# Kernel optimization log

Hardware: AMD Instinct MI355X
Metric: run time of the kernel (lower is better)

The kernel has to match this reference:

```python
import jax, jax.numpy as jnp
import numpy as np

EPS = 1e-08


def setup_inputs() -> dict:
    key = jax.random.key(0)
    k1, k2 = jax.random.split(key)
    n, d = 8192, 64
    x = jax.random.normal(k1, (n, d), dtype=jnp.float32)
    y = jax.random.randint(k2, (n,), 0, 10, dtype=jnp.int64)
    # weights = 1 / temperature_init = 1 / 0.1
    weights = jnp.full((1,), 10.0, dtype=jnp.float32)
    return {"x": x, "y": y, "weights": weights}


def reference(x, y, weights):
    n = x.shape[0]
    # pairwise euclidean distances (torch.cdist p=2)
    sq = jnp.sum(x * x, axis=1)                      # [n]
    d2 = sq[:, None] + sq[None, :] - 2.0 * (x @ x.T)  # [n,n]
    eye = jnp.eye(n, dtype=bool)
    d2 = jnp.maximum(d2, 0.0)
    dist = jnp.where(eye, 0.0, jnp.sqrt(jnp.where(eye, 1.0, d2)))  # safe sqrt on diag
    expo = jnp.exp(-dist * weights[0])               # [n,n]
    same = (y[:, None] == y[None, :]) & ~eye         # same-class, excluding self
    top = jnp.sum(jnp.where(same, expo, 0.0), axis=1)  # [n]
    bot = jnp.sum(jnp.where(~eye, expo, 0.0), axis=1)  # [n]
    fracs = jnp.log(top / (bot + EPS))
    loss = -jnp.mean(fracs)
    return loss
```

## Files before the change

### kernel.cpp

```cpp
#include <hip/hip_runtime.h>

typedef _Float16 f16x8 __attribute__((ext_vector_type(8)));
typedef float    f32x4 __attribute__((ext_vector_type(4)));

#define N_ROWS 8192
#define DIM 64
#define EPS 1e-8f
#define LOG2E 1.4426950408889634f
#define SHIFT 64.0f
#define SHIFT_LN 44.361419555836499802f
#define TILE_I 256
#define TILE_J 128
#define NTJ (TILE_J / 16)
#define NBI (N_ROWS / TILE_I)
#define TB (NBI * (NBI + 1))


__global__ void snn_prep(const float* __restrict__ x, _Float16* __restrict__ xh,
                         _Float16* __restrict__ xl, float* __restrict__ sq,
                         float* __restrict__ top, float* __restrict__ bot,
                         float* __restrict__ out) {
    const int gt = blockIdx.x * 256 + threadIdx.x;
    if (gt < N_ROWS) { top[gt] = 0.0f; bot[gt] = 0.0f; }
    if (gt == 0) out[0] = 0.0f;
    const int row = gt >> 6, lane = threadIdx.x & 63;
    float v = x[row * DIM + lane];
    _Float16 h = (_Float16)v;
    _Float16 l = (_Float16)(v - (float)h);
    xh[row * DIM + lane] = h;
    xl[row * DIM + lane] = l;
    float s = v * v;
    #pragma unroll
    for (int off = 32; off > 0; off >>= 1) s += __shfl_xor(s, off, 64);
    if (lane == 0) sq[row] = s;
}

__global__ __launch_bounds__(256, 2) void snn_mfma(
    const _Float16* __restrict__ xh, const _Float16* __restrict__ xl,
    const float* __restrict__ sq, const int* __restrict__ y,
    const float* __restrict__ w,
    float* __restrict__ top, float* __restrict__ bot)
{
    __shared__ float s_sqj[TILE_J];
    __shared__ int   s_yj[TILE_J];
    __shared__ float s_jt[4][TILE_J];
    __shared__ float s_jb[4][TILE_J];

    const int bid = blockIdx.x;
    int bi = (int)((sqrtf(4.0f * (float)bid + 1.0f) - 1.0f) * 0.5f);
    while ((bi + 1) * (bi + 2) <= bid) ++bi;
    while (bi * (bi + 1) > bid) --bi;
    const int bj = bid - bi * (bi + 1);
    const bool diag = (bj >= 2 * bi);
    const int I0 = bi * TILE_I, J0 = bj * TILE_J;

    const int tid = threadIdx.x, wv = tid >> 6, lane = tid & 63;
    const int mrow = lane & 15, kq = lane >> 4;

    if (tid < TILE_J) {
        s_sqj[tid] = sq[J0 + tid];
        s_yj[tid]  = y[J0 + tid];
    }
    __syncthreads();

    const int iw = I0 + wv * 64;

    f16x8 ah[4][2], al[4][2];
    #pragma unroll
    for (int mt = 0; mt < 4; mt++)
        #pragma unroll
        for (int kc = 0; kc < 2; kc++) {
            int a = (iw + mt * 16 + mrow) * DIM + kc * 32 + kq * 8;
            ah[mt][kc] = *(const f16x8*)(xh + a);
            al[mt][kc] = *(const f16x8*)(xl + a);
        }

    float sqi[4][4]; int ypack[4];
    #pragma unroll
    for (int mt = 0; mt < 4; mt++) {
        int yp = 0;
        #pragma unroll
        for (int rr = 0; rr < 4; rr++) {
            int i = iw + mt * 16 + kq * 4 + rr;
            sqi[mt][rr] = sq[i];
            yp |= (y[i] & 255) << (8 * rr);
        }
        ypack[mt] = yp;
    }

    float ts[4][4], bs[4][4];
    #pragma unroll
    for (int mt = 0; mt < 4; mt++)
        #pragma unroll
        for (int rr = 0; rr < 4; rr++) { ts[mt][rr] = 0.0f; bs[mt][rr] = 0.0f; }

    const float c1 = -w[0] * LOG2E;

#define LOAD_B_AND_MFMA(NT_)                                                     \
    const int jbase = J0 + (NT_) * 16;                                           \
    const int boff = (jbase + mrow) * DIM + kq * 8;                              \
    f16x8 bh0 = *(const f16x8*)(xh + boff);                                      \
    f16x8 bh1 = *(const f16x8*)(xh + boff + 32);                                 \
    f16x8 bl0 = *(const f16x8*)(xl + boff);                                      \
    f16x8 bl1 = *(const f16x8*)(xl + boff + 32);                                 \
    const float sqj = s_sqj[(NT_) * 16 + mrow];                                  \
    const int   yj  = s_yj[(NT_) * 16 + mrow];                                   \
    f32x4 acc[4];                                                                \
    _Pragma("unroll")                                                            \
    for (int mt = 0; mt < 4; mt++) acc[mt] = (f32x4){0.f, 0.f, 0.f, 0.f};        \
    _Pragma("unroll")                                                            \
    for (int mt = 0; mt < 4; mt++)                                               \
        acc[mt] = __builtin_amdgcn_mfma_f32_16x16x32_f16(ah[mt][0], bh0, acc[mt], 0, 0, 0); \
    _Pragma("unroll")                                                            \
    for (int mt = 0; mt < 4; mt++)                                               \
        acc[mt] = __builtin_amdgcn_mfma_f32_16x16x32_f16(ah[mt][1], bh1, acc[mt], 0, 0, 0); \
    _Pragma("unroll")                                                            \
    for (int mt = 0; mt < 4; mt++)                                               \
        acc[mt] = __builtin_amdgcn_mfma_f32_16x16x32_f16(ah[mt][0], bl0, acc[mt], 0, 0, 0); \
    _Pragma("unroll")                                                            \
    for (int mt = 0; mt < 4; mt++)                                               \
        acc[mt] = __builtin_amdgcn_mfma_f32_16x16x32_f16(ah[mt][1], bl1, acc[mt], 0, 0, 0); \
    _Pragma("unroll")                                                            \
    for (int mt = 0; mt < 4; mt++)                                               \
        acc[mt] = __builtin_amdgcn_mfma_f32_16x16x32_f16(al[mt][0], bh0, acc[mt], 0, 0, 0); \
    _Pragma("unroll")                                                            \
    for (int mt = 0; mt < 4; mt++)                                               \
        acc[mt] = __builtin_amdgcn_mfma_f32_16x16x32_f16(al[mt][1], bh1, acc[mt], 0, 0, 0);

    if (!diag) {
        for (int nt = 0; nt < NTJ; nt++) {
            LOAD_B_AND_MFMA(nt)
            float jt = 0.0f, jb = 0.0f;
            #pragma unroll
            for (int mt = 0; mt < 4; mt++)
                #pragma unroll
                for (int rr = 0; rr < 4; rr++) {
                    float d2 = fmaf(-2.0f, acc[mt][rr], sqi[mt][rr] + sqj);
                    d2 = fmaxf(d2, 0.0f);
                    float dist = __builtin_amdgcn_sqrtf(d2);
                    float e2 = exp2f(fmaf(c1, dist, SHIFT));
                    float e2t = (yj == ((ypack[mt] >> (8 * rr)) & 255)) ? e2 : 0.0f;
                    ts[mt][rr] += e2t;
                    bs[mt][rr] += e2;
                    jt += e2t;
                    jb += e2;
                }
            jt += __shfl_xor(jt, 16, 64); jt += __shfl_xor(jt, 32, 64);
            jb += __shfl_xor(jb, 16, 64); jb += __shfl_xor(jb, 32, 64);
            if (kq == 0) {
                s_jt[wv][nt * 16 + mrow] = jt;
                s_jb[wv][nt * 16 + mrow] = jb;
            }
        }
    } else {
        for (int nt = 0; nt < NTJ; nt++) {
            LOAD_B_AND_MFMA(nt)
            const int j = jbase + mrow;
            #pragma unroll
            for (int mt = 0; mt < 4; mt++)
                #pragma unroll
                for (int rr = 0; rr < 4; rr++) {
                    int i = iw + mt * 16 + kq * 4 + rr;
                    float d2 = fmaf(-2.0f, acc[mt][rr], sqi[mt][rr] + sqj);
                    d2 = fmaxf(d2, 0.0f);
                    float dist = __builtin_amdgcn_sqrtf(d2);
                    float e2 = exp2f(fmaf(c1, dist, SHIFT));
                    bool offd = (i != j);
                    bool same = offd && (yj == ((ypack[mt] >> (8 * rr)) & 255));
                    bs[mt][rr] += offd ? e2 : 0.0f;
                    ts[mt][rr] += same ? e2 : 0.0f;
                }
        }
    }
#undef LOAD_B_AND_MFMA

    #pragma unroll
    for (int mt = 0; mt < 4; mt++)
        #pragma unroll
        for (int rr = 0; rr < 4; rr++) {
            float tv = ts[mt][rr], bv = bs[mt][rr];
            #pragma unroll
            for (int off = 1; off < 16; off <<= 1) {
                tv += __shfl_xor(tv, off, 64);
                bv += __shfl_xor(bv, off, 64);
            }
            if (mrow == 0) {
                int i = iw + mt * 16 + kq * 4 + rr;
                atomicAdd(&top[i], tv);
                atomicAdd(&bot[i], bv);
            }
        }

    if (!diag) {
        __syncthreads();
        if (tid < TILE_J) {
            float t = s_jt[0][tid] + s_jt[1][tid] + s_jt[2][tid] + s_jt[3][tid];
            float b = s_jb[0][tid] + s_jb[1][tid] + s_jb[2][tid] + s_jb[3][tid];
            atomicAdd(&top[J0 + tid], t);
            atomicAdd(&bot[J0 + tid], b);
        }
    }
}

__global__ __launch_bounds__(256) void snn_final(
    const float* __restrict__ top, const float* __restrict__ bot,
    float* __restrict__ out)
{
    const int i = blockIdx.x * 256 + threadIdx.x;
    float t = top[i];
    float b = bot[i] * 0x1p-64f + EPS;
    float acc = (logf(t) - SHIFT_LN) - logf(b);
    #pragma unroll
    for (int off = 32; off > 0; off >>= 1) acc += __shfl_xor(acc, off, 64);
    __shared__ float red[4];
    if ((threadIdx.x & 63) == 0) red[threadIdx.x >> 6] = acc;
    __syncthreads();
    if (threadIdx.x == 0) {
        float s = red[0] + red[1] + red[2] + red[3];
        atomicAdd(out, -s / (float)N_ROWS);
    }
}

extern "C" void kernel_launch(void* const* d_in, const int* in_sizes, int n_in,
                              void* d_out, int out_size, void* d_ws, size_t ws_size,
                              hipStream_t stream) {
    const float* x = (const float*)d_in[0];
    const int*   y = (const int*)d_in[1];
    const float* w = (const float*)d_in[2];
    float* out = (float*)d_out;

    float* ws  = (float*)d_ws;
    float* top = ws;
    float* bot = ws + N_ROWS;
    float* sq  = ws + 2 * N_ROWS;
    _Float16* xh = (_Float16*)(ws + 3 * N_ROWS);
    _Float16* xl = xh + (size_t)N_ROWS * DIM;

    snn_prep<<<N_ROWS / 4, 256, 0, stream>>>(x, xh, xl, sq, top, bot, out);
    snn_mfma<<<TB, 256, 0, stream>>>(xh, xl, sq, y, w, top, bot);
    snn_final<<<N_ROWS / 256, 256, 0, stream>>>(top, bot, out);
}
```

Before: 117.3 us.

## Fuse final reduction via last-block counter, prefetch B tiles, use raw exp2

Removes the separate snn_final launch. The last block to finish the MFMA kernel, found through a global atomic counter, computes the log-ratio mean over all rows. It also software-prefetches the next B fragments in the off-diagonal loop and switches exp2f to the hardware builtin. This saves one kernel launch and hides some global load latency. In exchange it adds a threadfence per block, a serialized single-block tail reduction and more register pressure.

Result: slower. 269.5 us (+129.9%).

```diff
diff --git a/kernel.cpp b/kernel.cpp
--- a/kernel.cpp
+++ b/kernel.cpp
@@ -15,6 +15,8 @@
 #define NBI (N_ROWS / TILE_I)
 #define TB (NBI * (NBI + 1))
 
+__device__ unsigned int g_ctr;
+
 
 __global__ void snn_prep(const float* __restrict__ x, _Float16* __restrict__ xh,
                          _Float16* __restrict__ xl, float* __restrict__ sq,
@@ -22,7 +24,7 @@
                          float* __restrict__ out) {
     const int gt = blockIdx.x * 256 + threadIdx.x;
     if (gt < N_ROWS) { top[gt] = 0.0f; bot[gt] = 0.0f; }
-    if (gt == 0) out[0] = 0.0f;
+    if (gt == 0) { out[0] = 0.0f; g_ctr = 0u; }
     const int row = gt >> 6, lane = threadIdx.x & 63;
     float v = x[row * DIM + lane];
     _Float16 h = (_Float16)v;
@@ -39,12 +41,15 @@
     const _Float16* __restrict__ xh, const _Float16* __restrict__ xl,
     const float* __restrict__ sq, const int* __restrict__ y,
     const float* __restrict__ w,
-    float* __restrict__ top, float* __restrict__ bot)
+    float* __restrict__ top, float* __restrict__ bot,
+    float* __restrict__ out)
 {
     __shared__ float s_sqj[TILE_J];
     __shared__ int   s_yj[TILE_J];
     __shared__ float s_jt[4][TILE_J];
     __shared__ float s_jb[4][TILE_J];
+    __shared__ bool  s_last;
+    __shared__ float s_red[4];
 
     const int bid = blockIdx.x;
     int bi = (int)((sqrtf(4.0f * (float)bid + 1.0f) - 1.0f) * 0.5f);
@@ -96,40 +101,48 @@
 
     const float c1 = -w[0] * LOG2E;
 
-#define LOAD_B_AND_MFMA(NT_)                                                     \
-    const int jbase = J0 + (NT_) * 16;                                           \
-    const int boff = (jbase + mrow) * DIM + kq * 8;                              \
-    f16x8 bh0 = *(const f16x8*)(xh + boff);                                      \
-    f16x8 bh1 = *(const f16x8*)(xh + boff + 32);                                 \
-    f16x8 bl0 = *(const f16x8*)(xl + boff);                                      \
-    f16x8 bl1 = *(const f16x8*)(xl + boff + 32);                                 \
-    const float sqj = s_sqj[(NT_) * 16 + mrow];                                  \
-    const int   yj  = s_yj[(NT_) * 16 + mrow];                                   \
+#define DO_MFMA()                                                                \
     f32x4 acc[4];                                                                \
     _Pragma("unroll")                                                            \
     for (int mt = 0; mt < 4; mt++) acc[mt] = (f32x4){0.f, 0.f, 0.f, 0.f};        \
     _Pragma("unroll")                                                            \
     for (int mt = 0; mt < 4; mt++)                                               \
-        acc[mt] = __builtin_amdgcn_mfma_f32_16x16x32_f16(ah[mt][0], bh0, acc[mt], 0, 0, 0); \
-    _Pragma("unroll")                                                            \
-    for (int mt = 0; mt < 4; mt++)                                               \
-        acc[mt] = __builtin_amdgcn_mfma_f32_16x16x32_f16(ah[mt][1], bh1, acc[mt], 0, 0, 0); \
-    _Pragma("unroll")                                                            \
-    for (int mt = 0; mt < 4; mt++)                                               \
-        acc[mt] = __builtin_amdgcn_mfma_f32_16x16x32_f16(ah[mt][0], bl0, acc[mt], 0, 0, 0); \
-    _Pragma("unroll")                                                            \
-    for (int mt = 0; mt < 4; mt++)                                               \
-        acc[mt] = __builtin_amdgcn_mfma_f32_16x16x32_f16(ah[mt][1], bl1, acc[mt], 0, 0, 0); \
-    _Pragma("unroll")                                                            \
-    for (int mt = 0; mt < 4; mt++)                                               \
-        acc[mt] = __builtin_amdgcn_mfma_f32_16x16x32_f16(al[mt][0], bh0, acc[mt], 0, 0, 0); \
-    _Pragma("unroll")                                                            \
-    for (int mt = 0; mt < 4; mt++)                                               \
-        acc[mt] = __builtin_amdgcn_mfma_f32_16x16x32_f16(al[mt][1], bh1, acc[mt], 0, 0, 0);
+        acc[mt] = __builtin_amdgcn_mfma_f32_16x16x32_f16(ah[mt][0], cbh0, acc[mt], 0, 0, 0); \
+    _Pragma("unroll")                                                            \
+    for (int mt = 0; mt < 4; mt++)                                               \
+        acc[mt] = __builtin_amdgcn_mfma_f32_16x16x32_f16(ah[mt][1], cbh1, acc[mt], 0, 0, 0); \
+    _Pragma("unroll")                                                            \
+    for (int mt = 0; mt < 4; mt++)                                               \
+        acc[mt] = __builtin_amdgcn_mfma_f32_16x16x32_f16(ah[mt][0], cbl0, acc[mt], 0, 0, 0); \
+    _Pragma("unroll")                                                            \
+    for (int mt = 0; mt < 4; mt++)                                               \
+        acc[mt] = __builtin_amdgcn_mfma_f32_16x16x32_f16(ah[mt][1], cbl1, acc[mt], 0, 0, 0); \
+    _Pragma("unroll")                                                            \
+    for (int mt = 0; mt < 4; mt++)                                               \
+        acc[mt] = __builtin_amdgcn_mfma_f32_16x16x32_f16(al[mt][0], cbh0, acc[mt], 0, 0, 0); \
+    _Pragma("unroll")                                                            \
+    for (int mt = 0; mt < 4; mt++)                                               \
+        acc[mt] = __builtin_amdgcn_mfma_f32_16x16x32_f16(al[mt][1], cbh1, acc[mt], 0, 0, 0);
 
     if (!diag) {
+        int boff0 = (J0 + mrow) * DIM + kq * 8;
+        f16x8 cbh0 = *(const f16x8*)(xh + boff0);
+        f16x8 cbh1 = *(const f16x8*)(xh + boff0 + 32);
+        f16x8 cbl0 = *(const f16x8*)(xl + boff0);
+        f16x8 cbl1 = *(const f16x8*)(xl + boff0 + 32);
+        #pragma unroll
         for (int nt = 0; nt < NTJ; nt++) {
-            LOAD_B_AND_MFMA(nt)
+            f16x8 nbh0, nbh1, nbl0, nbl1;
+            if (nt + 1 < NTJ) {
+                int nb = (J0 + (nt + 1) * 16 + mrow) * DIM + kq * 8;
+                nbh0 = *(const f16x8*)(xh + nb);
+                nbh1 = *(const f16x8*)(xh + nb + 32);
+                nbl0 = *(const f16x8*)(xl + nb);
+                nbl1 = *(const f16x8*)(xl + nb + 32);
+            }
+            const float sqj = s_sqj[nt * 16 + mrow];
+            const int   yj  = s_yj[nt * 16 + mrow];
+            DO_MFMA()
             float jt = 0.0f, jb = 0.0f;
             #pragma unroll
             for (int mt = 0; mt < 4; mt++)
@@ -138,7 +151,7 @@
                     float d2 = fmaf(-2.0f, acc[mt][rr], sqi[mt][rr] + sqj);
                     d2 = fmaxf(d2, 0.0f);
                     float dist = __builtin_amdgcn_sqrtf(d2);
-                    float e2 = exp2f(fmaf(c1, dist, SHIFT));
+                    float e2 = __builtin_amdgcn_exp2f(fmaf(c1, dist, SHIFT));
                     float e2t = (yj == ((ypack[mt] >> (8 * rr)) & 255)) ? e2 : 0.0f;
                     ts[mt][rr] += e2t;
                     bs[mt][rr] += e2;
@@ -151,11 +164,20 @@
                 s_jt[wv][nt * 16 + mrow] = jt;
                 s_jb[wv][nt * 16 + mrow] = jb;
             }
+            if (nt + 1 < NTJ) { cbh0 = nbh0; cbh1 = nbh1; cbl0 = nbl0; cbl1 = nbl1; }
         }
     } else {
         for (int nt = 0; nt < NTJ; nt++) {
-            LOAD_B_AND_MFMA(nt)
-            const int j = jbase + mrow;
+            const int jbase = J0 + nt * 16;
+            const int boff = (jbase + mrow) * DIM + kq * 8;
+            f16x8 cbh0 = *(const f16x8*)(xh + boff);
+            f16x8 cbh1 = *(const f16x8*)(xh + boff + 32);
+            f16x8 cbl0 = *(const f16x8*)(xl + boff);
+            f16x8 cbl1 = *(const f16x8*)(xl + boff + 32);
+            const float sqj = s_sqj[nt * 16 + mrow];
+            const int   yj  = s_yj[nt * 16 + mrow];
+            const int   j   = jbase + mrow;
+            DO_MFMA()
             #pragma unroll
             for (int mt = 0; mt < 4; mt++)
                 #pragma unroll
@@ -164,7 +186,7 @@
                     float d2 = fmaf(-2.0f, acc[mt][rr], sqi[mt][rr] + sqj);
                     d2 = fmaxf(d2, 0.0f);
                     float dist = __builtin_amdgcn_sqrtf(d2);
-                    float e2 = exp2f(fmaf(c1, dist, SHIFT));
+                    float e2 = __builtin_amdgcn_exp2f(fmaf(c1, dist, SHIFT));
                     bool offd = (i != j);
                     bool same = offd && (yj == ((ypack[mt] >> (8 * rr)) & 255));
                     bs[mt][rr] += offd ? e2 : 0.0f;
@@ -172,7 +194,7 @@
                 }
         }
     }
-#undef LOAD_B_AND_MFMA
+#undef DO_MFMA
 
     #pragma unroll
     for (int mt = 0; mt < 4; mt++)
@@ -200,24 +222,24 @@
             atomicAdd(&bot[J0 + tid], b);
         }
     }
-}
-
-__global__ __launch_bounds__(256) void snn_final(
-    const float* __restrict__ top, const float* __restrict__ bot,
-    float* __restrict__ out)
-{
-    const int i = blockIdx.x * 256 + threadIdx.x;
-    float t = top[i];
-    float b = bot[i] * 0x1p-64f + EPS;
-    float acc = (logf(t) - SHIFT_LN) - logf(b);
-    #pragma unroll
-    for (int off = 32; off > 0; off >>= 1) acc += __shfl_xor(acc, off, 64);
-    __shared__ float red[4];
-    if ((threadIdx.x & 63) == 0) red[threadIdx.x >> 6] = acc;
+
+    __threadfence();
     __syncthreads();
-    if (threadIdx.x == 0) {
-        float s = red[0] + red[1] + red[2] + red[3];
-        atomicAdd(out, -s / (float)N_ROWS);
+    if (tid == 0) s_last = (atomicAdd(&g_ctr, 1u) == TB - 1);
+    __syncthreads();
+    if (s_last) {
+        float acc = 0.0f;
+        for (int r2 = tid; r2 < N_ROWS; r2 += 256) {
+            float t = __hip_atomic_load(&top[r2], __ATOMIC_RELAXED, __HIP_MEMORY_SCOPE_AGENT);
+            float b = __hip_atomic_load(&bot[r2], __ATOMIC_RELAXED, __HIP_MEMORY_SCOPE_AGENT);
+            acc += (logf(t) - SHIFT_LN) - logf(b * 0x1p-64f + EPS);
+        }
+        #pragma unroll
+        for (int off = 32; off > 0; off >>= 1) acc += __shfl_xor(acc, off, 64);
+        if ((tid & 63) == 0) s_red[tid >> 6] = acc;
+        __syncthreads();
+        if (tid == 0)
+            out[0] = -(s_red[0] + s_red[1] + s_red[2] + s_red[3]) / (float)N_ROWS;
     }
 }
 
@@ -237,6 +259,5 @@
     _Float16* xl = xh + (size_t)N_ROWS * DIM;
 
     snn_prep<<<N_ROWS / 4, 256, 0, stream>>>(x, xh, xl, sq, top, bot, out);
-    snn_mfma<<<TB, 256, 0, stream>>>(xh, xl, sq, y, w, top, bot);
-    snn_final<<<N_ROWS / 256, 256, 0, stream>>>(top, bot, out);
+    snn_mfma<<<TB, 256, 0, stream>>>(xh, xl, sq, y, w, top, bot, out);
 }
```

## Use square 256x256 off-diagonal tiles with split diagonal blocks and raw exp2

Applied to the files above, without the earlier changes.

Reworks the symmetric tile schedule: off-diagonal blocks now cover 256x256 tiles (16 column sub-tiles), and each diagonal 256-row band is split into two 128-column blocks. Fewer, larger blocks cut the per-block fixed cost of loading A fragments, sqi/y and the atomics, and improve reuse of the register-resident A operand. It also swaps exp2f for the raw hardware exp2 builtin to drop range-handling code. The trade-offs are fewer blocks, so possibly worse load balance and tail effects, and the host launch grid must match the new TB count.

After: 129.8 us. +10.7%, slower.

```diff
diff --git a/kernel.cpp b/kernel.cpp
--- a/kernel.cpp
+++ b/kernel.cpp
@@ -9,11 +9,10 @@
 #define LOG2E 1.4426950408889634f
 #define SHIFT 64.0f
 #define SHIFT_LN 44.361419555836499802f
-#define TILE_I 256
-#define TILE_J 128
-#define NTJ (TILE_J / 16)
-#define NBI (N_ROWS / TILE_I)
-#define TB (NBI * (NBI + 1))
+#define TILE 256
+#define NBI (N_ROWS / TILE)
+#define OFFB (NBI * (NBI - 1) / 2)
+#define TB (OFFB + 2 * NBI)
 
 
 __global__ void snn_prep(const float* __restrict__ x, _Float16* __restrict__ xh,
@@ -41,23 +40,31 @@
     const float* __restrict__ w,
     float* __restrict__ top, float* __restrict__ bot)
 {
-    __shared__ float s_sqj[TILE_J];
-    __shared__ int   s_yj[TILE_J];
-    __shared__ float s_jt[4][TILE_J];
-    __shared__ float s_jb[4][TILE_J];
+    __shared__ float s_sqj[TILE];
+    __shared__ int   s_yj[TILE];
+    __shared__ float s_jt[4][TILE];
+    __shared__ float s_jb[4][TILE];
 
     const int bid = blockIdx.x;
-    int bi = (int)((sqrtf(4.0f * (float)bid + 1.0f) - 1.0f) * 0.5f);
-    while ((bi + 1) * (bi + 2) <= bid) ++bi;
-    while (bi * (bi + 1) > bid) --bi;
-    const int bj = bid - bi * (bi + 1);
-    const bool diag = (bj >= 2 * bi);
-    const int I0 = bi * TILE_I, J0 = bj * TILE_J;
+    const bool diag = (bid >= OFFB);
+
+    int bi, I0, J0, NT;
+    if (!diag) {
+        bi = (int)((1.0f + sqrtf(8.0f * (float)bid + 1.0f)) * 0.5f);
+        while (bi * (bi - 1) / 2 > bid) --bi;
+        while ((bi + 1) * bi / 2 <= bid) ++bi;
+        const int bj = bid - bi * (bi - 1) / 2;
+        I0 = bi * TILE; J0 = bj * TILE; NT = 16;
+    } else {
+        const int t = bid - OFFB;
+        bi = t >> 1;
+        I0 = bi * TILE; J0 = bi * TILE + (t & 1) * 128; NT = 8;
+    }
 
     const int tid = threadIdx.x, wv = tid >> 6, lane = tid & 63;
     const int mrow = lane & 15, kq = lane >> 4;
 
-    if (tid < TILE_J) {
+    if (tid < NT * 16) {
         s_sqj[tid] = sq[J0 + tid];
         s_yj[tid]  = y[J0 + tid];
     }
@@ -96,40 +103,39 @@
 
     const float c1 = -w[0] * LOG2E;
 
-#define LOAD_B_AND_MFMA(NT_)                                                     \
-    const int jbase = J0 + (NT_) * 16;                                           \
-    const int boff = (jbase + mrow) * DIM + kq * 8;                              \
-    f16x8 bh0 = *(const f16x8*)(xh + boff);                                      \
-    f16x8 bh1 = *(const f16x8*)(xh + boff + 32);                                 \
-    f16x8 bl0 = *(const f16x8*)(xl + boff);                                      \
-    f16x8 bl1 = *(const f16x8*)(xl + boff + 32);                                 \
-    const float sqj = s_sqj[(NT_) * 16 + mrow];                                  \
-    const int   yj  = s_yj[(NT_) * 16 + mrow];                                   \
+#define LOAD_B_AND_MFMA()                                                        \
+    const int boff = (J0 + nt * 16 + mrow) * DIM + kq * 8;                       \
+    f16x8 cbh0 = *(const f16x8*)(xh + boff);                                     \
+    f16x8 cbh1 = *(const f16x8*)(xh + boff + 32);                                \
+    f16x8 cbl0 = *(const f16x8*)(xl + boff);                                     \
+    f16x8 cbl1 = *(const f16x8*)(xl + boff + 32);                                \
+    const float sqj = s_sqj[nt * 16 + mrow];                                     \
+    const int   yj  = s_yj[nt * 16 + mrow];                                      \
     f32x4 acc[4];                                                                \
     _Pragma("unroll")                                                            \
     for (int mt = 0; mt < 4; mt++) acc[mt] = (f32x4){0.f, 0.f, 0.f, 0.f};        \
     _Pragma("unroll")                                                            \
     for (int mt = 0; mt < 4; mt++)                                               \
-        acc[mt] = __builtin_amdgcn_mfma_f32_16x16x32_f16(ah[mt][0], bh0, acc[mt], 0, 0, 0); \
-    _Pragma("unroll")                                                            \
-    for (int mt = 0; mt < 4; mt++)                                               \
-        acc[mt] = __builtin_amdgcn_mfma_f32_16x16x32_f16(ah[mt][1], bh1, acc[mt], 0, 0, 0); \
-    _Pragma("unroll")                                                            \
-    for (int mt = 0; mt < 4; mt++)                                               \
-        acc[mt] = __builtin_amdgcn_mfma_f32_16x16x32_f16(ah[mt][0], bl0, acc[mt], 0, 0, 0); \
-    _Pragma("unroll")                                                            \
-    for (int mt = 0; mt < 4; mt++)                                               \
-        acc[mt] = __builtin_amdgcn_mfma_f32_16x16x32_f16(ah[mt][1], bl1, acc[mt], 0, 0, 0); \
-    _Pragma("unroll")                                                            \
-    for (int mt = 0; mt < 4; mt++)                                               \
-        acc[mt] = __builtin_amdgcn_mfma_f32_16x16x32_f16(al[mt][0], bh0, acc[mt], 0, 0, 0); \
-    _Pragma("unroll")                                                            \
-    for (int mt = 0; mt < 4; mt++)                                               \
-        acc[mt] = __builtin_amdgcn_mfma_f32_16x16x32_f16(al[mt][1], bh1, acc[mt], 0, 0, 0);
+        acc[mt] = __builtin_amdgcn_mfma_f32_16x16x32_f16(ah[mt][0], cbh0, acc[mt], 0, 0, 0); \
+    _Pragma("unroll")                                                            \
+    for (int mt = 0; mt < 4; mt++)                                               \
+        acc[mt] = __builtin_amdgcn_mfma_f32_16x16x32_f16(ah[mt][1], cbh1, acc[mt], 0, 0, 0); \
+    _Pragma("unroll")                                                            \
+    for (int mt = 0; mt < 4; mt++)                                               \
+        acc[mt] = __builtin_amdgcn_mfma_f32_16x16x32_f16(ah[mt][0], cbl0, acc[mt], 0, 0, 0); \
+    _Pragma("unroll")                                                            \
+    for (int mt = 0; mt < 4; mt++)                                               \
+        acc[mt] = __builtin_amdgcn_mfma_f32_16x16x32_f16(ah[mt][1], cbl1, acc[mt], 0, 0, 0); \
+    _Pragma("unroll")                                                            \
+    for (int mt = 0; mt < 4; mt++)                                               \
+        acc[mt] = __builtin_amdgcn_mfma_f32_16x16x32_f16(al[mt][0], cbh0, acc[mt], 0, 0, 0); \
+    _Pragma("unroll")                                                            \
+    for (int mt = 0; mt < 4; mt++)                                               \
+        acc[mt] = __builtin_amdgcn_mfma_f32_16x16x32_f16(al[mt][1], cbh1, acc[mt], 0, 0, 0);
 
     if (!diag) {
-        for (int nt = 0; nt < NTJ; nt++) {
-            LOAD_B_AND_MFMA(nt)
+        for (int nt = 0; nt < 16; nt++) {
+            LOAD_B_AND_MFMA()
             float jt = 0.0f, jb = 0.0f;
             #pragma unroll
             for (int mt = 0; mt < 4; mt++)
@@ -138,7 +144,7 @@
                     float d2 = fmaf(-2.0f, acc[mt][rr], sqi[mt][rr] + sqj);
                     d2 = fmaxf(d2, 0.0f);
                     float dist = __builtin_amdgcn_sqrtf(d2);
-                    float e2 = exp2f(fmaf(c1, dist, SHIFT));
+                    float e2 = __builtin_amdgcn_exp2f(fmaf(c1, dist, SHIFT));
                     float e2t = (yj == ((ypack[mt] >> (8 * rr)) & 255)) ? e2 : 0.0f;
                     ts[mt][rr] += e2t;
                     bs[mt][rr] += e2;
@@ -153,9 +159,9 @@
             }
         }
     } else {
-        for (int nt = 0; nt < NTJ; nt++) {
-            LOAD_B_AND_MFMA(nt)
-            const int j = jbase + mrow;
+        for (int nt = 0; nt < 8; nt++) {
+            LOAD_B_AND_MFMA()
+            const int j = J0 + nt * 16 + mrow;
             #pragma unroll
             for (int mt = 0; mt < 4; mt++)
                 #pragma unroll
@@ -164,7 +170,7 @@
                     float d2 = fmaf(-2.0f, acc[mt][rr], sqi[mt][rr] + sqj);
                     d2 = fmaxf(d2, 0.0f);
                     float dist = __builtin_amdgcn_sqrtf(d2);
-                    float e2 = exp2f(fmaf(c1, dist, SHIFT));
+                    float e2 = __builtin_amdgcn_exp2f(fmaf(c1, dist, SHIFT));
                     bool offd = (i != j);
                     bool same = offd && (yj == ((ypack[mt] >> (8 * rr)) & 255));
                     bs[mt][rr] += offd ? e2 : 0.0f;
@@ -193,12 +199,10 @@
 
     if (!diag) {
         __syncthreads();
-        if (tid < TILE_J) {
-            float t = s_jt[0][tid] + s_jt[1][tid] + s_jt[2][tid] + s_jt[3][tid];
-            float b = s_jb[0][tid] + s_jb[1][tid] + s_jb[2][tid] + s_jb[3][tid];
-            atomicAdd(&top[J0 + tid], t);
-            atomicAdd(&bot[J0 + tid], b);
-        }
+        float t = s_jt[0][tid] + s_jt[1][tid] + s_jt[2][tid] + s_jt[3][tid];
+        float b = s_jb[0][tid] + s_jb[1][tid] + s_jb[2][tid] + s_jb[3][tid];
+        atomicAdd(&top[J0 + tid], t);
+        atomicAdd(&bot[J0 + tid], b);
     }
 }
 
```
